# Kernel tuning notes

Measured on AMD Instinct MI355X. Metric: run time of the kernel, lower is better.

## Reference

```python
import jax, jax.numpy as jnp
import numpy as np

VOCAB = 50001; W2V = 300; S2V = 256; HID = 256; COUT = 256; NTAG = 4; NHEADS = 5
N_POSTS = 2048; SEQ = 64


def mha(x, wqkv, bqkv, wo, bo, h):
    # torch nn.MultiheadAttention (batch_first, eval mode, no mask)
    n, s, d = x.shape
    hd = d // h
    qkv = x @ wqkv.T + bqkv                      # [n, s, 3d]
    q, k, v = jnp.split(qkv, 3, axis=-1)
    rs = lambda t: t.reshape(n, s, h, hd).transpose(0, 2, 1, 3)  # [n, h, s, hd]
    q, k, v = rs(q), rs(k), rs(v)
    att = jax.nn.softmax(jnp.einsum('nhqd,nhkd->nhqk', q, k) * (hd ** -0.5), axis=-1)
    o = jnp.einsum('nhqk,nhkd->nhqd', att, v).transpose(0, 2, 1, 3).reshape(n, s, d)
    return o @ wo.T + bo


def gcn_conv(x, ei, w, b):
    n = x.shape[0]
    loops = jnp.arange(n)
    src = jnp.concatenate([ei[0], loops])
    dst = jnp.concatenate([ei[1], loops])
    deg = jax.ops.segment_sum(jnp.ones(dst.shape[0], dtype=x.dtype), dst, num_segments=n)
    dinv = jnp.where(deg > 0, jax.lax.rsqrt(deg), 0.0)
    norm = dinv[src] * dinv[dst]                 # [E+n]
    h = x @ w.T                                  # [n, out]
    return jax.ops.segment_sum(norm[:, None] * h[src], dst, num_segments=n) + b


def gcn_branch(x, ei, root, w1, b1, w2, b2):
    # GCN.forward: conv1 -> cat root feat -> relu -> conv2 -> relu -> cat conv1 root -> mean
    n = x.shape[0]
    c1 = gcn_conv(x, ei, w1, b1)                 # [n, HID]
    post_root = jnp.broadcast_to(x[root], (n, x.shape[1]))
    c2_in = jax.nn.relu(jnp.concatenate([c1, post_root], axis=1))
    c2 = jax.nn.relu(gcn_conv(c2_in, ei, w2, b2))
    c1_root = jnp.broadcast_to(c1[root], (n, c1.shape[1]))
    feat = jnp.concatenate([c1_root, c2], axis=1)  # [n, HID+COUT]
    return jnp.mean(feat, axis=0).reshape(1, -1)


def setup_inputs() -> dict:
    key = jax.random.key(0)
    ks = jax.random.split(key, 16)
    p = lambda i, shp, sc=0.02: jax.random.normal(ks[i], shp, dtype=jnp.float32) * sc
    return {
        'nodeText': jax.random.randint(ks[0], (N_POSTS, SEQ), 0, VOCAB),
        'edgeIndexTD': jax.random.randint(ks[1], (2, N_POSTS - 1), 0, N_POSTS),
        'edgeIndexBU': jax.random.randint(ks[2], (2, N_POSTS - 1), 0, N_POSTS),
        'threadIndex': 0,
        'mission': 1,
        'embed_w': p(3, (VOCAB, W2V), 1.0),
        'in_proj_w': p(4, (3 * W2V, W2V)),
        'in_proj_b': jnp.zeros((3 * W2V,), jnp.float32),
        'out_proj_w': p(5, (W2V, W2V)),
        'out_proj_b': jnp.zeros((W2V,), jnp.float32),
        's2v_w': p(6, (S2V, W2V)),
        's2v_b': jnp.zeros((S2V,), jnp.float32),
        'td_w1': p(7, (HID, S2V)), 'td_b1': jnp.zeros((HID,), jnp.float32),
        'td_w2': p(8, (COUT, HID + S2V)), 'td_b2': jnp.zeros((COUT,), jnp.float32),
        'bu_w1': p(9, (HID, S2V)), 'bu_b1': jnp.zeros((HID,), jnp.float32),
        'bu_w2': p(10, (COUT, HID + S2V)), 'bu_b2': jnp.zeros((COUT,), jnp.float32),
        'fc_w': p(11, (NTAG, (COUT + HID) * 2)),
        'fc_b': jnp.zeros((NTAG,), jnp.float32),
    }


def reference(nodeText, edgeIndexTD, edgeIndexBU, threadIndex, mission,
              embed_w, in_proj_w, in_proj_b, out_proj_w, out_proj_b,
              s2v_w, s2v_b, td_w1, td_b1, td_w2, td_b2,
              bu_w1, bu_b1, bu_w2, bu_b2, fc_w, fc_b):
    # ABGCN.forward, mission == 1 (rumor/BiGCN path), eval mode (dropout off)
    nf = embed_w[nodeText]                                  # [N, S, W2V]
    nf = mha(nf, in_proj_w, in_proj_b, out_proj_w, out_proj_b, NHEADS)
    nf = jnp.tanh(nf @ s2v_w.T + s2v_b)                     # [N, S, S2V]
    s2v = nf[:, 0, :]                                       # first token per post
    td = gcn_branch(s2v, edgeIndexTD, threadIndex, td_w1, td_b1, td_w2, td_b2)
    bu = gcn_branch(s2v, edgeIndexBU, threadIndex, bu_w1, bu_b1, bu_w2, bu_b2)
    return jnp.concatenate([td, bu], axis=1) @ fc_w.T + fc_b  # [1, NTAG]
```

## Files before the change

kernel.cpp:

```cpp
#include <hip/hip_runtime.h>

#define NPOSTS 2048
#define SEQ 64
#define W2V 300
#define NH 5
#define HD 60
#define S2VD 256
#define HIDD 256
#define NEDGE 2047
#define UDIM (NH * W2V)

__device__ __forceinline__ float dot4(float4 a, float4 b) {
    return fmaf(a.x, b.x, fmaf(a.y, b.y, fmaf(a.z, b.z, a.w * b.w)));
}

__global__ __launch_bounds__(320) void k_qu(
    const int* __restrict__ nodeText, const float* __restrict__ embed_w,
    const float* __restrict__ Wqkv, const float* __restrict__ bqkv,
    float* __restrict__ uout)
{
    const int r0 = blockIdx.x * 4;
    const int tid = threadIdx.x;
    __shared__ float sE[4][W2V];
    __shared__ float sQ[4][W2V];

    if (tid < 300) {
        int r = tid / 75, c4 = (tid % 75) * 4;
        int t = nodeText[(size_t)(r0 + r) * SEQ];
        const float4 v = *reinterpret_cast<const float4*>(embed_w + (size_t)t * W2V + c4);
        sE[r][c4] = v.x; sE[r][c4 + 1] = v.y; sE[r][c4 + 2] = v.z; sE[r][c4 + 3] = v.w;
    }
    __syncthreads();

    if (tid < W2V) {
        const float* wr = Wqkv + (size_t)tid * W2V;
        float b = bqkv[tid];
        float a0 = b, a1 = b, a2 = b, a3 = b;
        for (int c = 0; c < W2V; ++c) {
            float wv = wr[c];
            a0 = fmaf(wv, sE[0][c], a0);
            a1 = fmaf(wv, sE[1][c], a1);
            a2 = fmaf(wv, sE[2][c], a2);
            a3 = fmaf(wv, sE[3][c], a3);
        }
        sQ[0][tid] = a0; sQ[1][tid] = a1; sQ[2][tid] = a2; sQ[3][tid] = a3;
    }
    __syncthreads();

    if (tid < W2V) {
        for (int h = 0; h < NH; ++h) {
            const float* wb = Wqkv + (size_t)(W2V + h * HD) * W2V + tid;
            const float* q0 = &sQ[0][h * HD];
            const float* q1 = &sQ[1][h * HD];
            const float* q2 = &sQ[2][h * HD];
            const float* q3 = &sQ[3][h * HD];
            float a0 = 0.f, a1 = 0.f, a2 = 0.f, a3 = 0.f;
            for (int d = 0; d < HD; ++d) {
                float wv = wb[(size_t)d * W2V];
                a0 = fmaf(wv, q0[d], a0);
                a1 = fmaf(wv, q1[d], a1);
                a2 = fmaf(wv, q2[d], a2);
                a3 = fmaf(wv, q3[d], a3);
            }
            uout[(size_t)(r0 + 0) * UDIM + h * W2V + tid] = a0;
            uout[(size_t)(r0 + 1) * UDIM + h * W2V + tid] = a1;
            uout[(size_t)(r0 + 2) * UDIM + h * W2V + tid] = a2;
            uout[(size_t)(r0 + 3) * UDIM + h * W2V + tid] = a3;
        }
    }
}

__global__ __launch_bounds__(320) void k_att(
    const int* __restrict__ nodeText, const float* __restrict__ embed_w,
    float* __restrict__ ue)
{
    __shared__ int   stoks[SEQ];
    __shared__ float ssc[NH * SEQ];
    __shared__ float part[4][75][21];

    const int p = blockIdx.x;
    const int tid = threadIdx.x;
    const int wave = tid >> 6, lane = tid & 63;

    if (tid < SEQ) stoks[tid] = nodeText[p * SEQ + tid];
    __syncthreads();

    const float4* su4 = reinterpret_cast<const float4*>(ue + (size_t)p * UDIM);
    float4 u00 = su4[0 * 75 + lane];
    float4 u01 = su4[1 * 75 + lane];
    float4 u02 = su4[2 * 75 + lane];
    float4 u03 = su4[3 * 75 + lane];
    float4 u04 = su4[4 * 75 + lane];
    float4 z = make_float4(0.f, 0.f, 0.f, 0.f);
    float4 u10 = z, u11 = z, u12 = z, u13 = z, u14 = z;
    if (lane < 11) {
        u10 = su4[0 * 75 + 64 + lane];
        u11 = su4[1 * 75 + 64 + lane];
        u12 = su4[2 * 75 + 64 + lane];
        u13 = su4[3 * 75 + 64 + lane];
        u14 = su4[4 * 75 + 64 + lane];
    }

    const float SC = 0.12909944487358056f;
    for (int j = wave; j < SEQ; j += 5) {
        const float4* er = reinterpret_cast<const float4*>(embed_w + (size_t)stoks[j] * W2V);
        const float4 a = er[lane];
        float4 bb = z;
        if (lane < 11) bb = er[64 + lane];
        float s0 = dot4(a, u00) + dot4(bb, u10);
        float s1 = dot4(a, u01) + dot4(bb, u11);
        float s2 = dot4(a, u02) + dot4(bb, u12);
        float s3 = dot4(a, u03) + dot4(bb, u13);
        float s4 = dot4(a, u04) + dot4(bb, u14);
        #pragma unroll
        for (int off = 32; off > 0; off >>= 1) {
            s0 += __shfl_xor(s0, off);
            s1 += __shfl_xor(s1, off);
            s2 += __shfl_xor(s2, off);
            s3 += __shfl_xor(s3, off);
            s4 += __shfl_xor(s4, off);
        }
        if (lane == 0) {
            ssc[0 * SEQ + j] = s0 * SC;
            ssc[1 * SEQ + j] = s1 * SC;
            ssc[2 * SEQ + j] = s2 * SC;
            ssc[3 * SEQ + j] = s3 * SC;
            ssc[4 * SEQ + j] = s4 * SC;
        }
    }
    __syncthreads();

    {
        float v = ssc[wave * SEQ + lane];
        float m = v;
        #pragma unroll
        for (int off = 32; off > 0; off >>= 1) m = fmaxf(m, __shfl_xor(m, off));
        float e = expf(v - m);
        float s = e;
        #pragma unroll
        for (int off = 32; off > 0; off >>= 1) s += __shfl_xor(s, off);
        ssc[wave * SEQ + lane] = e / s;
    }
    __syncthreads();

    if (tid < 300) {
        const int c4 = tid % 75, g = tid / 75;
        float4 a0 = z, a1 = z, a2 = z, a3 = z, a4 = z;
        for (int jj = 0; jj < 16; ++jj) {
            int j = g * 16 + jj;
            const float4 em = *reinterpret_cast<const float4*>(
                embed_w + (size_t)stoks[j] * W2V + c4 * 4);
            float w0 = ssc[0 * SEQ + j], w1 = ssc[1 * SEQ + j], w2 = ssc[2 * SEQ + j];
            float w3 = ssc[3 * SEQ + j], w4 = ssc[4 * SEQ + j];
            a0.x = fmaf(w0, em.x, a0.x); a0.y = fmaf(w0, em.y, a0.y); a0.z = fmaf(w0, em.z, a0.z); a0.w = fmaf(w0, em.w, a0.w);
            a1.x = fmaf(w1, em.x, a1.x); a1.y = fmaf(w1, em.y, a1.y); a1.z = fmaf(w1, em.z, a1.z); a1.w = fmaf(w1, em.w, a1.w);
            a2.x = fmaf(w2, em.x, a2.x); a2.y = fmaf(w2, em.y, a2.y); a2.z = fmaf(w2, em.z, a2.z); a2.w = fmaf(w2, em.w, a2.w);
            a3.x = fmaf(w3, em.x, a3.x); a3.y = fmaf(w3, em.y, a3.y); a3.z = fmaf(w3, em.z, a3.z); a3.w = fmaf(w3, em.w, a3.w);
            a4.x = fmaf(w4, em.x, a4.x); a4.y = fmaf(w4, em.y, a4.y); a4.z = fmaf(w4, em.z, a4.z); a4.w = fmaf(w4, em.w, a4.w);
        }
        float* pp = &part[g][c4][0];
        pp[0] = a0.x; pp[1] = a0.y; pp[2] = a0.z; pp[3] = a0.w;
        pp[4] = a1.x; pp[5] = a1.y; pp[6] = a1.z; pp[7] = a1.w;
        pp[8] = a2.x; pp[9] = a2.y; pp[10] = a2.z; pp[11] = a2.w;
        pp[12] = a3.x; pp[13] = a3.y; pp[14] = a3.z; pp[15] = a3.w;
        pp[16] = a4.x; pp[17] = a4.y; pp[18] = a4.z; pp[19] = a4.w;
    }
    __syncthreads();

    float4* eo = reinterpret_cast<float4*>(ue + (size_t)p * UDIM);
    for (int o = tid; o < 375; o += 320) {
        int h = o / 75, c4 = o % 75;
        float x = 0.f, y = 0.f, zz = 0.f, w = 0.f;
        #pragma unroll
        for (int g = 0; g < 4; ++g) {
            const float* pp = &part[g][c4][h * 4];
            x += pp[0]; y += pp[1]; zz += pp[2]; w += pp[3];
        }
        eo[o] = make_float4(x, y, zz, w);
    }
}

__global__ __launch_bounds__(320) void k_oms(
    const float* __restrict__ e, const float* __restrict__ Wqkv, const float* __restrict__ bqkv,
    const float* __restrict__ Wo, const float* __restrict__ bo,
    const float* __restrict__ Ws, const float* __restrict__ bs,
    float* __restrict__ s2v_out)
{
    const int r0 = blockIdx.x * 4;
    const int tid = threadIdx.x;
    __shared__ float se[4][UDIM];
    __shared__ float so[4][W2V];
    __shared__ float sm[4][W2V];

    for (int i = tid; i < 4 * 375; i += 320) {
        int r = i / 375, c4 = (i % 375) * 4;
        const float4 v = *reinterpret_cast<const float4*>(e + (size_t)(r0 + r) * UDIM + c4);
        se[r][c4] = v.x; se[r][c4 + 1] = v.y; se[r][c4 + 2] = v.z; se[r][c4 + 3] = v.w;
    }
    __syncthreads();

    if (tid < W2V) {
        const int h = tid / HD;
        const float* wr = Wqkv + (size_t)(2 * W2V + tid) * W2V;
        float b = bqkv[2 * W2V + tid];
        float a0 = b, a1 = b, a2 = b, a3 = b;
        const float* e0 = &se[0][h * W2V];
        const float* e1 = &se[1][h * W2V];
        const float* e2 = &se[2][h * W2V];
        const float* e3 = &se[3][h * W2V];
        for (int c = 0; c < W2V; ++c) {
            float wv = wr[c];
            a0 = fmaf(wv, e0[c], a0);
            a1 = fmaf(wv, e1[c], a1);
            a2 = fmaf(wv, e2[c], a2);
            a3 = fmaf(wv, e3[c], a3);
        }
        so[0][tid] = a0; so[1][tid] = a1; so[2][tid] = a2; so[3][tid] = a3;
    }
    __syncthreads();

    if (tid < W2V) {
        const float* wr = Wo + (size_t)tid * W2V;
        float b = bo[tid];
        float a0 = b, a1 = b, a2 = b, a3 = b;
        for (int c = 0; c < W2V; ++c) {
            float wv = wr[c];
            a0 = fmaf(wv, so[0][c], a0);
            a1 = fmaf(wv, so[1][c], a1);
            a2 = fmaf(wv, so[2][c], a2);
            a3 = fmaf(wv, so[3][c], a3);
        }
        sm[0][tid] = a0; sm[1][tid] = a1; sm[2][tid] = a2; sm[3][tid] = a3;
    }
    __syncthreads();

    if (tid < S2VD) {
        const float* wr = Ws + (size_t)tid * W2V;
        float b = bs[tid];
        float a0 = b, a1 = b, a2 = b, a3 = b;
        for (int c = 0; c < W2V; ++c) {
            float wv = wr[c];
            a0 = fmaf(wv, sm[0][c], a0);
            a1 = fmaf(wv, sm[1][c], a1);
            a2 = fmaf(wv, sm[2][c], a2);
            a3 = fmaf(wv, sm[3][c], a3);
        }
        s2v_out[(size_t)(r0 + 0) * S2VD + tid] = tanhf(a0);
        s2v_out[(size_t)(r0 + 1) * S2VD + tid] = tanhf(a1);
        s2v_out[(size_t)(r0 + 2) * S2VD + tid] = tanhf(a2);
        s2v_out[(size_t)(r0 + 3) * S2VD + tid] = tanhf(a3);
    }
}


__global__ __launch_bounds__(256) void k_deg(
    const int* __restrict__ eiTD, const int* __restrict__ eiBU, int* __restrict__ deg)
{
    const int b = blockIdx.y;
    const int* ei = b ? eiBU : eiTD;
    int e = blockIdx.x * 256 + threadIdx.x;
    if (e < NEDGE) atomicAdd(&deg[b * NPOSTS + ei[NEDGE + e]], 1);
}

__global__ __launch_bounds__(256) void k_gemm1(
    const float* __restrict__ x, const float* __restrict__ wtd, const float* __restrict__ wbu,
    const float* __restrict__ btd, const float* __restrict__ bbu, const int* __restrict__ deg,
    float* __restrict__ hout, float* __restrict__ cout_)
{
    const int b = blockIdx.y;
    const float* w = b ? wbu : wtd;
    const float* bias = b ? bbu : btd;
    float* hb = hout + (size_t)b * NPOSTS * HIDD;
    float* cb = cout_ + (size_t)b * NPOSTS * HIDD;
    const int* dg = deg + b * NPOSTS;
    const int r0 = blockIdx.x * 16;
    const int tid = threadIdx.x;
    __shared__ float sx[16][S2VD];
    for (int i = tid; i < 16 * S2VD; i += 256)
        sx[i / S2VD][i % S2VD] = x[(size_t)(r0 + i / S2VD) * S2VD + (i % S2VD)];
    __syncthreads();
    float acc[16];
    #pragma unroll
    for (int r = 0; r < 16; ++r) acc[r] = 0.f;
    const float* wr = w + (size_t)tid * S2VD;
    for (int c = 0; c < S2VD; ++c) {
        float wv = wr[c];
        #pragma unroll
        for (int r = 0; r < 16; ++r) acc[r] = fmaf(wv, sx[r][c], acc[r]);
    }
    float bv = bias[tid];
    #pragma unroll
    for (int r = 0; r < 16; ++r) {
        int n = r0 + r;
        float dinv = 1.f / (float)(dg[n] + 1);
        hb[(size_t)n * HIDD + tid] = acc[r];
        cb[(size_t)n * HIDD + tid] = bv + acc[r] * dinv;
    }
}

__global__ __launch_bounds__(256) void k_gemm2(
    const float* __restrict__ c1, const float* __restrict__ w2td, const float* __restrict__ w2bu,
    const float* __restrict__ btd, const float* __restrict__ bbu, const int* __restrict__ deg,
    const float* __restrict__ rootv, float* __restrict__ hout, float* __restrict__ cout_)
{
    const int b = blockIdx.y;
    const float* w = b ? w2bu : w2td;
    const float* bias = b ? bbu : btd;
    const float* xin = c1 + (size_t)b * NPOSTS * HIDD;
    float* hb = hout + (size_t)b * NPOSTS * HIDD;
    float* cb = cout_ + (size_t)b * NPOSTS * HIDD;
    const int* dg = deg + b * NPOSTS;
    const int r0 = blockIdx.x * 16;
    const int tid = threadIdx.x;
    __shared__ float sx[16][HIDD];
    for (int i = tid; i < 16 * HIDD; i += 256)
        sx[i / HIDD][i % HIDD] = fmaxf(xin[(size_t)(r0 + i / HIDD) * HIDD + (i % HIDD)], 0.f);
    __syncthreads();
    float acc[16];
    const float rv = rootv[b * HIDD + tid];
    #pragma unroll
    for (int r = 0; r < 16; ++r) acc[r] = rv;
    const float* wr = w + (size_t)tid * 512;
    for (int c = 0; c < HIDD; ++c) {
        float wv = wr[c];
        #pragma unroll
        for (int r = 0; r < 16; ++r) acc[r] = fmaf(wv, sx[r][c], acc[r]);
    }
    float bv = bias[tid];
    #pragma unroll
    for (int r = 0; r < 16; ++r) {
        int n = r0 + r;
        float dinv = 1.f / (float)(dg[n] + 1);
        hb[(size_t)n * HIDD + tid] = acc[r];
        cb[(size_t)n * HIDD + tid] = bv + acc[r] * dinv;
    }
}

__global__ __launch_bounds__(256) void k_scat(
    const int* __restrict__ eiTD, const int* __restrict__ eiBU,
    const float* __restrict__ h, const int* __restrict__ deg, float* __restrict__ cacc)
{
    const int b = blockIdx.y, e = blockIdx.x, tid = threadIdx.x;
    const int* ei = b ? eiBU : eiTD;
    const int s = ei[e], d = ei[NEDGE + e];
    const int* dg = deg + b * NPOSTS;
    float norm = rsqrtf((float)(dg[s] + 1)) * rsqrtf((float)(dg[d] + 1));
    const float* hb = h + (size_t)b * NPOSTS * HIDD;
    float* cb = cacc + (size_t)b * NPOSTS * HIDD;
    atomicAdd(&cb[(size_t)d * HIDD + tid], norm * hb[(size_t)s * HIDD + tid]);
}

__global__ __launch_bounds__(256) void k_root(
    const float* __restrict__ s2v, const float* __restrict__ c1,
    const float* __restrict__ w2td, const float* __restrict__ w2bu,
    const int* __restrict__ rootPtr, float* __restrict__ rootv, float* __restrict__ c1root)
{
    const int b = blockIdx.y, tid = threadIdx.x;
    const float* w2 = b ? w2bu : w2td;
    const int root = rootPtr[0];
    __shared__ float sx[S2VD];
    sx[tid] = fmaxf(s2v[(size_t)root * S2VD + tid], 0.f);
    __syncthreads();
    const float* cb = c1 + (size_t)b * NPOSTS * HIDD;
    c1root[b * HIDD + tid] = cb[(size_t)root * HIDD + tid];
    const float* wr = w2 + (size_t)tid * 512 + 256;
    float acc = 0.f;
    #pragma unroll 4
    for (int c = 0; c < S2VD; ++c) acc = fmaf(wr[c], sx[c], acc);
    rootv[b * HIDD + tid] = acc;
}

__global__ __launch_bounds__(256) void k_reduce(
    const float* __restrict__ cacc, float* __restrict__ msum)
{
    const int b = blockIdx.y, tid = threadIdx.x;
    const int base = blockIdx.x * 32;
    const float* cb = cacc + (size_t)b * NPOSTS * HIDD;
    float local = 0.f;
    #pragma unroll 4
    for (int r = 0; r < 32; ++r) local += fmaxf(cb[(size_t)(base + r) * HIDD + tid], 0.f);
    atomicAdd(&msum[b * HIDD + tid], local);
}

__global__ __launch_bounds__(256) void k_final(
    const float* __restrict__ c1root, const float* __restrict__ msum,
    const float* __restrict__ fc_w, const float* __restrict__ fc_b, float* __restrict__ outp)
{
    const int tid = threadIdx.x;
    __shared__ float sf[1024];
    for (int k = tid; k < 1024; k += 256) {
        int seg = k >> 8, idx = k & 255;
        float v;
        if (seg == 0)      v = c1root[idx];
        else if (seg == 1) v = msum[idx] * (1.f / (float)NPOSTS);
        else if (seg == 2) v = c1root[256 + idx];
        else               v = msum[256 + idx] * (1.f / (float)NPOSTS);
        sf[k] = v;
    }
    __syncthreads();
    const int t = tid >> 6, lane = tid & 63;
    float part = 0.f;
    for (int k = lane; k < 1024; k += 64) part = fmaf(fc_w[t * 1024 + k], sf[k], part);
    #pragma unroll
    for (int off = 32; off > 0; off >>= 1) part += __shfl_down(part, off);
    if (lane == 0) outp[t] = part + fc_b[t];
}

extern "C" void kernel_launch(void* const* d_in, const int* in_sizes, int n_in,
                              void* d_out, int out_size, void* d_ws, size_t ws_size,
                              hipStream_t stream) {
    (void)in_sizes; (void)n_in; (void)out_size; (void)ws_size;

    const int*   nodeText   = (const int*)d_in[0];
    const int*   eiTD       = (const int*)d_in[1];
    const int*   eiBU       = (const int*)d_in[2];
    const int*   threadIdxP = (const int*)d_in[3];
    const float* embed_w    = (const float*)d_in[5];
    const float* in_proj_w  = (const float*)d_in[6];
    const float* in_proj_b  = (const float*)d_in[7];
    const float* out_proj_w = (const float*)d_in[8];
    const float* out_proj_b = (const float*)d_in[9];
    const float* s2v_w      = (const float*)d_in[10];
    const float* s2v_b      = (const float*)d_in[11];
    const float* td_w1      = (const float*)d_in[12];
    const float* td_b1      = (const float*)d_in[13];
    const float* td_w2      = (const float*)d_in[14];
    const float* td_b2      = (const float*)d_in[15];
    const float* bu_w1      = (const float*)d_in[16];
    const float* bu_b1      = (const float*)d_in[17];
    const float* bu_w2      = (const float*)d_in[18];
    const float* bu_b2      = (const float*)d_in[19];
    const float* fc_w       = (const float*)d_in[20];
    const float* fc_b       = (const float*)d_in[21];
    float* outp = (float*)d_out;

    char* w = (char*)d_ws;
    int*   deg    = (int*)w;
    float* msum   = (float*)(w + 16384);
    float* rootv  = (float*)(w + 16384 + 2048);
    float* c1root = (float*)(w + 16384 + 4096);
    float* s2v    = (float*)(w + 24576);
    float* hbuf   = (float*)(w + 24576 + 2097152);
    float* cbuf   = (float*)(w + 24576 + 2097152 + 4194304);
    float* uebuf  = (float*)(w + 24576 + 2097152 + 4194304 + 4194304);

    hipMemsetAsync(d_ws, 0, 16384 + 2048, stream);

    k_deg<<<dim3((NEDGE + 255) / 256, 2), 256, 0, stream>>>(eiTD, eiBU, deg);

    k_qu <<<NPOSTS / 4, 320, 0, stream>>>(nodeText, embed_w, in_proj_w, in_proj_b, uebuf);
    k_att<<<NPOSTS, 320, 0, stream>>>(nodeText, embed_w, uebuf);
    k_oms<<<NPOSTS / 4, 320, 0, stream>>>(uebuf, in_proj_w, in_proj_b,
                                          out_proj_w, out_proj_b, s2v_w, s2v_b, s2v);

    k_gemm1<<<dim3(NPOSTS / 16, 2), 256, 0, stream>>>(s2v, td_w1, bu_w1, td_b1, bu_b1, deg,
                                                      hbuf, cbuf);
    k_scat<<<dim3(NEDGE, 2), 256, 0, stream>>>(eiTD, eiBU, hbuf, deg, cbuf);

    k_root<<<dim3(1, 2), 256, 0, stream>>>(s2v, cbuf, td_w2, bu_w2, threadIdxP, rootv, c1root);

    k_gemm2<<<dim3(NPOSTS / 16, 2), 256, 0, stream>>>(cbuf, td_w2, bu_w2, td_b2, bu_b2, deg,
                                                      rootv, hbuf, cbuf);
    k_scat<<<dim3(NEDGE, 2), 256, 0, stream>>>(eiTD, eiBU, hbuf, deg, cbuf);

    k_reduce<<<dim3(NPOSTS / 32, 2), 256, 0, stream>>>(cbuf, msum);

    k_final<<<1, 256, 0, stream>>>(c1root, msum, fc_w, fc_b, outp);
}
```

Before: 289.8 us.

## Fold out_proj into s2v weights, restructure attention kernel, vectorize GEMM weight loads

A new prologue kernel precomputes Ws·Wo and a folded bias, so the per-post out-projection and s2v layers collapse into one 300→256 matmul, removing a full 300×300 stage per row. The attention kernel now handles two posts per 256-thread block, splitting the score dot products and the weighted sum across wave halves with shared-memory staging. Weight and shared-memory reads in k_qu, k_oms and both GCN GEMMs are switched to float4. The folded weights are stored in hbuf before it is reused, and the reassociated sums shift floating-point rounding slightly.

```diff
diff --git a/kernel.cpp b/kernel.cpp
--- a/kernel.cpp
+++ b/kernel.cpp
@@ -14,6 +14,31 @@
     return fmaf(a.x, b.x, fmaf(a.y, b.y, fmaf(a.z, b.z, a.w * b.w)));
 }
 
+__global__ __launch_bounds__(256) void k_wfold(
+    const float* __restrict__ Ws, const float* __restrict__ Wo,
+    const float* __restrict__ bo, const float* __restrict__ bs,
+    float* __restrict__ WsWo, float* __restrict__ bias2)
+{
+    const int cb = blockIdx.x;
+    const int t = threadIdx.x;
+    const float* wsr = Ws + (size_t)t * W2V;
+    float4 acc = make_float4(0.f, 0.f, 0.f, 0.f);
+    for (int k = 0; k < W2V; ++k) {
+        float wv = wsr[k];
+        const float4 wo4 = *reinterpret_cast<const float4*>(Wo + (size_t)k * W2V + cb * 4);
+        acc.x = fmaf(wv, wo4.x, acc.x);
+        acc.y = fmaf(wv, wo4.y, acc.y);
+        acc.z = fmaf(wv, wo4.z, acc.z);
+        acc.w = fmaf(wv, wo4.w, acc.w);
+    }
+    *reinterpret_cast<float4*>(WsWo + (size_t)t * W2V + cb * 4) = acc;
+    if (cb == 0) {
+        float b = bs[t];
+        for (int k = 0; k < W2V; ++k) b = fmaf(wsr[k], bo[k], b);
+        bias2[t] = b;
+    }
+}
+
 __global__ __launch_bounds__(320) void k_qu(
     const int* __restrict__ nodeText, const float* __restrict__ embed_w,
     const float* __restrict__ Wqkv, const float* __restrict__ bqkv,
@@ -33,15 +58,24 @@
     __syncthreads();
 
     if (tid < W2V) {
-        const float* wr = Wqkv + (size_t)tid * W2V;
+        const float4* wr4 = reinterpret_cast<const float4*>(Wqkv + (size_t)tid * W2V);
+        const float4* e0 = reinterpret_cast<const float4*>(&sE[0][0]);
+        const float4* e1 = reinterpret_cast<const float4*>(&sE[1][0]);
+        const float4* e2 = reinterpret_cast<const float4*>(&sE[2][0]);
+        const float4* e3 = reinterpret_cast<const float4*>(&sE[3][0]);
         float b = bqkv[tid];
         float a0 = b, a1 = b, a2 = b, a3 = b;
-        for (int c = 0; c < W2V; ++c) {
-            float wv = wr[c];
-            a0 = fmaf(wv, sE[0][c], a0);
-            a1 = fmaf(wv, sE[1][c], a1);
-            a2 = fmaf(wv, sE[2][c], a2);
-            a3 = fmaf(wv, sE[3][c], a3);
+        for (int c4 = 0; c4 < 75; ++c4) {
+            float4 w4 = wr4[c4];
+            float4 v0 = e0[c4], v1 = e1[c4], v2 = e2[c4], v3 = e3[c4];
+            a0 = fmaf(w4.x, v0.x, a0); a1 = fmaf(w4.x, v1.x, a1);
+            a2 = fmaf(w4.x, v2.x, a2); a3 = fmaf(w4.x, v3.x, a3);
+            a0 = fmaf(w4.y, v0.y, a0); a1 = fmaf(w4.y, v1.y, a1);
+            a2 = fmaf(w4.y, v2.y, a2); a3 = fmaf(w4.y, v3.y, a3);
+            a0 = fmaf(w4.z, v0.z, a0); a1 = fmaf(w4.z, v1.z, a1);
+            a2 = fmaf(w4.z, v2.z, a2); a3 = fmaf(w4.z, v3.z, a3);
+            a0 = fmaf(w4.w, v0.w, a0); a1 = fmaf(w4.w, v1.w, a1);
+            a2 = fmaf(w4.w, v2.w, a2); a3 = fmaf(w4.w, v3.w, a3);
         }
         sQ[0][tid] = a0; sQ[1][tid] = a1; sQ[2][tid] = a2; sQ[3][tid] = a3;
     }
@@ -70,180 +104,183 @@
     }
 }
 
-__global__ __launch_bounds__(320) void k_att(
+__global__ __launch_bounds__(256) void k_att(
     const int* __restrict__ nodeText, const float* __restrict__ embed_w,
     float* __restrict__ ue)
 {
-    __shared__ int   stoks[SEQ];
-    __shared__ float ssc[NH * SEQ];
-    __shared__ float part[4][75][21];
-
-    const int p = blockIdx.x;
+    __shared__ float su[2][UDIM];
+    __shared__ int   stoks[2][SEQ];
+    __shared__ float sp[2][2][NH][SEQ];
+    __shared__ float satt[2][NH][SEQ];
+
+    const int p0 = blockIdx.x * 2;
     const int tid = threadIdx.x;
     const int wave = tid >> 6, lane = tid & 63;
-
-    if (tid < SEQ) stoks[tid] = nodeText[p * SEQ + tid];
-    __syncthreads();
-
-    const float4* su4 = reinterpret_cast<const float4*>(ue + (size_t)p * UDIM);
-    float4 u00 = su4[0 * 75 + lane];
-    float4 u01 = su4[1 * 75 + lane];
-    float4 u02 = su4[2 * 75 + lane];
-    float4 u03 = su4[3 * 75 + lane];
-    float4 u04 = su4[4 * 75 + lane];
-    float4 z = make_float4(0.f, 0.f, 0.f, 0.f);
-    float4 u10 = z, u11 = z, u12 = z, u13 = z, u14 = z;
-    if (lane < 11) {
-        u10 = su4[0 * 75 + 64 + lane];
-        u11 = su4[1 * 75 + 64 + lane];
-        u12 = su4[2 * 75 + 64 + lane];
-        u13 = su4[3 * 75 + 64 + lane];
-        u14 = su4[4 * 75 + 64 + lane];
-    }
-
-    const float SC = 0.12909944487358056f;
-    for (int j = wave; j < SEQ; j += 5) {
-        const float4* er = reinterpret_cast<const float4*>(embed_w + (size_t)stoks[j] * W2V);
-        const float4 a = er[lane];
-        float4 bb = z;
-        if (lane < 11) bb = er[64 + lane];
-        float s0 = dot4(a, u00) + dot4(bb, u10);
-        float s1 = dot4(a, u01) + dot4(bb, u11);
-        float s2 = dot4(a, u02) + dot4(bb, u12);
-        float s3 = dot4(a, u03) + dot4(bb, u13);
-        float s4 = dot4(a, u04) + dot4(bb, u14);
+    const int wp = wave >> 1;
+    const int wh = wave & 1;
+
+    if (tid < 2 * SEQ) stoks[tid >> 6][tid & 63] = nodeText[(size_t)(p0 + (tid >> 6)) * SEQ + (tid & 63)];
+    {
+        const float4* g = reinterpret_cast<const float4*>(ue + (size_t)p0 * UDIM);
+        float4* s = reinterpret_cast<float4*>(&su[0][0]);
+        for (int i = tid; i < 2 * UDIM / 4; i += 256) s[i] = g[i];
+    }
+    __syncthreads();
+
+    {
+        const int tok = stoks[wp][lane];
+        const float4* er = reinterpret_cast<const float4*>(embed_w + (size_t)tok * W2V);
+        const float4* u4 = reinterpret_cast<const float4*>(&su[wp][0]);
+        float a0 = 0.f, a1 = 0.f, a2 = 0.f, a3 = 0.f, a4 = 0.f;
+        const int c40 = wh ? 38 : 0, c41 = wh ? 75 : 38;
+        for (int c4 = c40; c4 < c41; ++c4) {
+            float4 ev = er[c4];
+            a0 += dot4(ev, u4[0 * 75 + c4]);
+            a1 += dot4(ev, u4[1 * 75 + c4]);
+            a2 += dot4(ev, u4[2 * 75 + c4]);
+            a3 += dot4(ev, u4[3 * 75 + c4]);
+            a4 += dot4(ev, u4[4 * 75 + c4]);
+        }
+        sp[wp][wh][0][lane] = a0;
+        sp[wp][wh][1][lane] = a1;
+        sp[wp][wh][2][lane] = a2;
+        sp[wp][wh][3][lane] = a3;
+        sp[wp][wh][4][lane] = a4;
+    }
+    __syncthreads();
+
+    if (wh == 0) {
+        const float SC = 0.12909944487358056f;
         #pragma unroll
-        for (int off = 32; off > 0; off >>= 1) {
-            s0 += __shfl_xor(s0, off);
-            s1 += __shfl_xor(s1, off);
-            s2 += __shfl_xor(s2, off);
-            s3 += __shfl_xor(s3, off);
-            s4 += __shfl_xor(s4, off);
-        }
-        if (lane == 0) {
-            ssc[0 * SEQ + j] = s0 * SC;
-            ssc[1 * SEQ + j] = s1 * SC;
-            ssc[2 * SEQ + j] = s2 * SC;
-            ssc[3 * SEQ + j] = s3 * SC;
-            ssc[4 * SEQ + j] = s4 * SC;
+        for (int h = 0; h < NH; ++h) {
+            float v = (sp[wp][0][h][lane] + sp[wp][1][h][lane]) * SC;
+            float m = v;
+            #pragma unroll
+            for (int off = 32; off > 0; off >>= 1) m = fmaxf(m, __shfl_xor(m, off));
+            float e = expf(v - m);
+            float s = e;
+            #pragma unroll
+            for (int off = 32; off > 0; off >>= 1) s += __shfl_xor(s, off);
+            satt[wp][h][lane] = e / s;
         }
     }
     __syncthreads();
 
     {
-        float v = ssc[wave * SEQ + lane];
-        float m = v;
-        #pragma unroll
-        for (int off = 32; off > 0; off >>= 1) m = fmaxf(m, __shfl_xor(m, off));
-        float e = expf(v - m);
-        float s = e;
-        #pragma unroll
-        for (int off = 32; off > 0; off >>= 1) s += __shfl_xor(s, off);
-        ssc[wave * SEQ + lane] = e / s;
-    }
-    __syncthreads();
-
-    if (tid < 300) {
-        const int c4 = tid % 75, g = tid / 75;
-        float4 a0 = z, a1 = z, a2 = z, a3 = z, a4 = z;
-        for (int jj = 0; jj < 16; ++jj) {
-            int j = g * 16 + jj;
-            const float4 em = *reinterpret_cast<const float4*>(
-                embed_w + (size_t)stoks[j] * W2V + c4 * 4);
-            float w0 = ssc[0 * SEQ + j], w1 = ssc[1 * SEQ + j], w2 = ssc[2 * SEQ + j];
-            float w3 = ssc[3 * SEQ + j], w4 = ssc[4 * SEQ + j];
-            a0.x = fmaf(w0, em.x, a0.x); a0.y = fmaf(w0, em.y, a0.y); a0.z = fmaf(w0, em.z, a0.z); a0.w = fmaf(w0, em.w, a0.w);
-            a1.x = fmaf(w1, em.x, a1.x); a1.y = fmaf(w1, em.y, a1.y); a1.z = fmaf(w1, em.z, a1.z); a1.w = fmaf(w1, em.w, a1.w);
-            a2.x = fmaf(w2, em.x, a2.x); a2.y = fmaf(w2, em.y, a2.y); a2.z = fmaf(w2, em.z, a2.z); a2.w = fmaf(w2, em.w, a2.w);
-            a3.x = fmaf(w3, em.x, a3.x); a3.y = fmaf(w3, em.y, a3.y); a3.z = fmaf(w3, em.z, a3.z); a3.w = fmaf(w3, em.w, a3.w);
-            a4.x = fmaf(w4, em.x, a4.x); a4.y = fmaf(w4, em.y, a4.y); a4.z = fmaf(w4, em.z, a4.z); a4.w = fmaf(w4, em.w, a4.w);
-        }
-        float* pp = &part[g][c4][0];
-        pp[0] = a0.x; pp[1] = a0.y; pp[2] = a0.z; pp[3] = a0.w;
-        pp[4] = a1.x; pp[5] = a1.y; pp[6] = a1.z; pp[7] = a1.w;
-        pp[8] = a2.x; pp[9] = a2.y; pp[10] = a2.z; pp[11] = a2.w;
-        pp[12] = a3.x; pp[13] = a3.y; pp[14] = a3.z; pp[15] = a3.w;
-        pp[16] = a4.x; pp[17] = a4.y; pp[18] = a4.z; pp[19] = a4.w;
-    }
-    __syncthreads();
-
-    float4* eo = reinterpret_cast<float4*>(ue + (size_t)p * UDIM);
-    for (int o = tid; o < 375; o += 320) {
-        int h = o / 75, c4 = o % 75;
-        float x = 0.f, y = 0.f, zz = 0.f, w = 0.f;
-        #pragma unroll
-        for (int g = 0; g < 4; ++g) {
-            const float* pp = &part[g][c4][h * 4];
-            x += pp[0]; y += pp[1]; zz += pp[2]; w += pp[3];
-        }
-        eo[o] = make_float4(x, y, zz, w);
+        const float4 z = make_float4(0.f, 0.f, 0.f, 0.f);
+        float4 accA[NH] = {z, z, z, z, z};
+        float4 accT[NH] = {z, z, z, z, z};
+        const bool tail = lane < 11;
+        const int j0 = wh * 32;
+        for (int jj = 0; jj < 32; ++jj) {
+            int j = j0 + jj;
+            const float4* er = reinterpret_cast<const float4*>(embed_w + (size_t)stoks[wp][j] * W2V);
+            float4 ea = er[lane];
+            float4 eb = tail ? er[64 + lane] : z;
+            #pragma unroll
+            for (int h = 0; h < NH; ++h) {
+                float av = satt[wp][h][j];
+                accA[h].x = fmaf(av, ea.x, accA[h].x);
+                accA[h].y = fmaf(av, ea.y, accA[h].y);
+                accA[h].z = fmaf(av, ea.z, accA[h].z);
+                accA[h].w = fmaf(av, ea.w, accA[h].w);
+                accT[h].x = fmaf(av, eb.x, accT[h].x);
+                accT[h].y = fmaf(av, eb.y, accT[h].y);
+                accT[h].z = fmaf(av, eb.z, accT[h].z);
+                accT[h].w = fmaf(av, eb.w, accT[h].w);
+            }
+        }
+        float4* ep = reinterpret_cast<float4*>(&su[wp][0]);
+        if (wh == 1) {
+            #pragma unroll
+            for (int h = 0; h < NH; ++h) ep[h * 75 + lane] = accA[h];
+            if (tail) {
+                #pragma unroll
+                for (int h = 0; h < NH; ++h) ep[h * 75 + 64 + lane] = accT[h];
+            }
+        }
+        __syncthreads();
+        if (wh == 0) {
+            float4* eo = reinterpret_cast<float4*>(ue + (size_t)(p0 + wp) * UDIM);
+            #pragma unroll
+            for (int h = 0; h < NH; ++h) {
+                float4 o = ep[h * 75 + lane];
+                o.x += accA[h].x; o.y += accA[h].y; o.z += accA[h].z; o.w += accA[h].w;
+                eo[h * 75 + lane] = o;
+            }
+            if (tail) {
+                #pragma unroll
+                for (int h = 0; h < NH; ++h) {
+                    float4 o = ep[h * 75 + 64 + lane];
+                    o.x += accT[h].x; o.y += accT[h].y; o.z += accT[h].z; o.w += accT[h].w;
+                    eo[h * 75 + 64 + lane] = o;
+                }
+            }
+        }
     }
 }
 
 __global__ __launch_bounds__(320) void k_oms(
     const float* __restrict__ e, const float* __restrict__ Wqkv, const float* __restrict__ bqkv,
-    const float* __restrict__ Wo, const float* __restrict__ bo,
-    const float* __restrict__ Ws, const float* __restrict__ bs,
+    const float* __restrict__ WsWo, const float* __restrict__ bias2,
     float* __restrict__ s2v_out)
 {
     const int r0 = blockIdx.x * 4;
     const int tid = threadIdx.x;
     __shared__ float se[4][UDIM];
     __shared__ float so[4][W2V];
-    __shared__ float sm[4][W2V];
-
-    for (int i = tid; i < 4 * 375; i += 320) {
-        int r = i / 375, c4 = (i % 375) * 4;
-        const float4 v = *reinterpret_cast<const float4*>(e + (size_t)(r0 + r) * UDIM + c4);
-        se[r][c4] = v.x; se[r][c4 + 1] = v.y; se[r][c4 + 2] = v.z; se[r][c4 + 3] = v.w;
+
+    {
+        const float4* g = reinterpret_cast<const float4*>(e + (size_t)r0 * UDIM);
+        float4* s = reinterpret_cast<float4*>(&se[0][0]);
+        for (int i = tid; i < 4 * UDIM / 4; i += 320) s[i] = g[i];
     }
     __syncthreads();
 
     if (tid < W2V) {
         const int h = tid / HD;
-        const float* wr = Wqkv + (size_t)(2 * W2V + tid) * W2V;
+        const float4* wr4 = reinterpret_cast<const float4*>(Wqkv + (size_t)(2 * W2V + tid) * W2V);
+        const float4* e0 = reinterpret_cast<const float4*>(&se[0][h * W2V]);
+        const float4* e1 = reinterpret_cast<const float4*>(&se[1][h * W2V]);
+        const float4* e2 = reinterpret_cast<const float4*>(&se[2][h * W2V]);
+        const float4* e3 = reinterpret_cast<const float4*>(&se[3][h * W2V]);
         float b = bqkv[2 * W2V + tid];
         float a0 = b, a1 = b, a2 = b, a3 = b;
-        const float* e0 = &se[0][h * W2V];
-        const float* e1 = &se[1][h * W2V];
-        const float* e2 = &se[2][h * W2V];
-        const float* e3 = &se[3][h * W2V];
-        for (int c = 0; c < W2V; ++c) {
-            float wv = wr[c];
-            a0 = fmaf(wv, e0[c], a0);
-            a1 = fmaf(wv, e1[c], a1);
-            a2 = fmaf(wv, e2[c], a2);
-            a3 = fmaf(wv, e3[c], a3);
+        for (int c4 = 0; c4 < 75; ++c4) {
+            float4 w4 = wr4[c4];
+            float4 v0 = e0[c4], v1 = e1[c4], v2 = e2[c4], v3 = e3[c4];
+            a0 = fmaf(w4.x, v0.x, a0); a1 = fmaf(w4.x, v1.x, a1);
+            a2 = fmaf(w4.x, v2.x, a2); a3 = fmaf(w4.x, v3.x, a3);
+            a0 = fmaf(w4.y, v0.y, a0); a1 = fmaf(w4.y, v1.y, a1);
+            a2 = fmaf(w4.y, v2.y, a2); a3 = fmaf(w4.y, v3.y, a3);
+            a0 = fmaf(w4.z, v0.z, a0); a1 = fmaf(w4.z, v1.z, a1);
+            a2 = fmaf(w4.z, v2.z, a2); a3 = fmaf(w4.z, v3.z, a3);
+            a0 = fmaf(w4.w, v0.w, a0); a1 = fmaf(w4.w, v1.w, a1);
+            a2 = fmaf(w4.w, v2.w, a2); a3 = fmaf(w4.w, v3.w, a3);
         }
         so[0][tid] = a0; so[1][tid] = a1; so[2][tid] = a2; so[3][tid] = a3;
     }
     __syncthreads();
 
-    if (tid < W2V) {
-        const float* wr = Wo + (size_t)tid * W2V;
-        float b = bo[tid];
+    if (tid < S2VD) {
+        const float4* wr4 = reinterpret_cast<const float4*>(WsWo + (size_t)tid * W2V);
+        const float4* o0 = reinterpret_cast<const float4*>(&so[0][0]);
+        const float4* o1 = reinterpret_cast<const float4*>(&so[1][0]);
+        const float4* o2 = reinterpret_cast<const float4*>(&so[2][0]);
+        const float4* o3 = reinterpret_cast<const float4*>(&so[3][0]);
+        float b = bias2[tid];
         float a0 = b, a1 = b, a2 = b, a3 = b;
-        for (int c = 0; c < W2V; ++c) {
-            float wv = wr[c];
-            a0 = fmaf(wv, so[0][c], a0);
-            a1 = fmaf(wv, so[1][c], a1);
-            a2 = fmaf(wv, so[2][c], a2);
-            a3 = fmaf(wv, so[3][c], a3);
-        }
-        sm[0][tid] = a0; sm[1][tid] = a1; sm[2][tid] = a2; sm[3][tid] = a3;
-    }
-    __syncthreads();
-
-    if (tid < S2VD) {
-        const float* wr = Ws + (size_t)tid * W2V;
-        float b = bs[tid];
-        float a0 = b, a1 = b, a2 = b, a3 = b;
-        for (int c = 0; c < W2V; ++c) {
-            float wv = wr[c];
-            a0 = fmaf(wv, sm[0][c], a0);
-            a1 = fmaf(wv, sm[1][c], a1);
-            a2 = fmaf(wv, sm[2][c], a2);
-            a3 = fmaf(wv, sm[3][c], a3);
+        for (int c4 = 0; c4 < 75; ++c4) {
+            float4 w4 = wr4[c4];
+            float4 v0 = o0[c4], v1 = o1[c4], v2 = o2[c4], v3 = o3[c4];
+            a0 = fmaf(w4.x, v0.x, a0); a1 = fmaf(w4.x, v1.x, a1);
+            a2 = fmaf(w4.x, v2.x, a2); a3 = fmaf(w4.x, v3.x, a3);
+            a0 = fmaf(w4.y, v0.y, a0); a1 = fmaf(w4.y, v1.y, a1);
+            a2 = fmaf(w4.y, v2.y, a2); a3 = fmaf(w4.y, v3.y, a3);
+            a0 = fmaf(w4.z, v0.z, a0); a1 = fmaf(w4.z, v1.z, a1);
+            a2 = fmaf(w4.z, v2.z, a2); a3 = fmaf(w4.z, v3.z, a3);
+            a0 = fmaf(w4.w, v0.w, a0); a1 = fmaf(w4.w, v1.w, a1);
+            a2 = fmaf(w4.w, v2.w, a2); a3 = fmaf(w4.w, v3.w, a3);
         }
         s2v_out[(size_t)(r0 + 0) * S2VD + tid] = tanhf(a0);
         s2v_out[(size_t)(r0 + 1) * S2VD + tid] = tanhf(a1);
@@ -282,11 +319,17 @@
     float acc[16];
     #pragma unroll
     for (int r = 0; r < 16; ++r) acc[r] = 0.f;
-    const float* wr = w + (size_t)tid * S2VD;
-    for (int c = 0; c < S2VD; ++c) {
-        float wv = wr[c];
+    const float4* wr4 = reinterpret_cast<const float4*>(w + (size_t)tid * S2VD);
+    for (int c4 = 0; c4 < 64; ++c4) {
+        float4 w4 = wr4[c4];
         #pragma unroll
-        for (int r = 0; r < 16; ++r) acc[r] = fmaf(wv, sx[r][c], acc[r]);
+        for (int r = 0; r < 16; ++r) {
+            const float4 v = *reinterpret_cast<const float4*>(&sx[r][c4 * 4]);
+            acc[r] = fmaf(w4.x, v.x, acc[r]);
+            acc[r] = fmaf(w4.y, v.y, acc[r]);
+            acc[r] = fmaf(w4.z, v.z, acc[r]);
+            acc[r] = fmaf(w4.w, v.w, acc[r]);
+        }
     }
     float bv = bias[tid];
     #pragma unroll
@@ -320,11 +363,17 @@
     const float rv = rootv[b * HIDD + tid];
     #pragma unroll
     for (int r = 0; r < 16; ++r) acc[r] = rv;
-    const float* wr = w + (size_t)tid * 512;
-    for (int c = 0; c < HIDD; ++c) {
-        float wv = wr[c];
+    const float4* wr4 = reinterpret_cast<const float4*>(w + (size_t)tid * 512);
+    for (int c4 = 0; c4 < 64; ++c4) {
+        float4 w4 = wr4[c4];
         #pragma unroll
-        for (int r = 0; r < 16; ++r) acc[r] = fmaf(wv, sx[r][c], acc[r]);
+        for (int r = 0; r < 16; ++r) {
+            const float4 v = *reinterpret_cast<const float4*>(&sx[r][c4 * 4]);
+            acc[r] = fmaf(w4.x, v.x, acc[r]);
+            acc[r] = fmaf(w4.y, v.y, acc[r]);
+            acc[r] = fmaf(w4.z, v.z, acc[r]);
+            acc[r] = fmaf(w4.w, v.w, acc[r]);
+        }
     }
     float bv = bias[tid];
     #pragma unroll
@@ -444,14 +493,17 @@
     float* cbuf   = (float*)(w + 24576 + 2097152 + 4194304);
     float* uebuf  = (float*)(w + 24576 + 2097152 + 4194304 + 4194304);
 
+    float* WsWo  = hbuf;
+    float* bias2 = hbuf + S2VD * W2V;
+
     hipMemsetAsync(d_ws, 0, 16384 + 2048, stream);
 
     k_deg<<<dim3((NEDGE + 255) / 256, 2), 256, 0, stream>>>(eiTD, eiBU, deg);
+    k_wfold<<<75, 256, 0, stream>>>(s2v_w, out_proj_w, out_proj_b, s2v_b, WsWo, bias2);
 
     k_qu <<<NPOSTS / 4, 320, 0, stream>>>(nodeText, embed_w, in_proj_w, in_proj_b, uebuf);
-    k_att<<<NPOSTS, 320, 0, stream>>>(nodeText, embed_w, uebuf);
-    k_oms<<<NPOSTS / 4, 320, 0, stream>>>(uebuf, in_proj_w, in_proj_b,
-                                          out_proj_w, out_proj_b, s2v_w, s2v_b, s2v);
+    k_att<<<NPOSTS / 2, 256, 0, stream>>>(nodeText, embed_w, uebuf);
+    k_oms<<<NPOSTS / 4, 320, 0, stream>>>(uebuf, in_proj_w, in_proj_b, WsWo, bias2, s2v);
 
     k_gemm1<<<dim3(NPOSTS / 16, 2), 256, 0, stream>>>(s2v, td_w1, bu_w1, td_b1, bu_b1, deg,
                                                       hbuf, cbuf);
```

Result: slower. 314.2 us (+8.4%).
